# Kernel optimization log

Hardware: AMD Instinct MI355X
Metric: run time of the kernel (lower is better)

## Reference

```python
import jax, jax.numpy as jnp
import numpy as np

NUM_HEADS = 16
HEAD_DIM = 128  # hidden_size 2048 / 16 heads


def setup_inputs() -> dict:
    key = jax.random.key(0)
    k1, k2, k3 = jax.random.split(key, 3)
    bsz, seq, hidden = 2, 2048, 2048
    return {
        "query": jax.random.normal(k1, (bsz, seq, hidden), dtype=jnp.float32),
        "key": jax.random.normal(k2, (bsz, seq, hidden), dtype=jnp.float32),
        "value": jax.random.normal(k3, (bsz, seq, hidden), dtype=jnp.float32),
        "attention_mask": jnp.zeros((1, 1, seq, seq), dtype=jnp.float32),
    }


def reference(query, key, value, attention_mask):
    bsz, seq, hidden = query.shape
    h, d = NUM_HEADS, HEAD_DIM
    # (b, s, h*d) -> (b, h, s, d)
    q = query.reshape(bsz, seq, h, d).transpose(0, 2, 1, 3)
    k = key.reshape(bsz, seq, h, d).transpose(0, 2, 1, 3)
    v = value.reshape(bsz, seq, h, d).transpose(0, 2, 1, 3)
    # scores: (b, h, s, s)
    scores = jnp.einsum("bhqd,bhkd->bhqk", q, k) / jnp.sqrt(jnp.float32(d))
    scores = scores + attention_mask
    probs = jax.nn.softmax(scores.astype(jnp.float32), axis=-1).astype(q.dtype)
    out = jnp.einsum("bhqk,bhkd->bhqd", probs, v)
    # (b, h, s, d) -> (b, s, h*d)
    return out.transpose(0, 2, 1, 3).reshape(bsz, seq, hidden)
```

## Files before the change

### kernel.cpp

```cpp
#include <hip/hip_runtime.h>
#include <hip/hip_bf16.h>
#include <math.h>

#define SEQ 2048
#define NH 16
#define HD 128
#define HID 2048
#define KVB 64
#define NKT (SEQ/KVB)
#define QB 128
#define QBLK 64

typedef __attribute__((ext_vector_type(8))) short bf16x8;
typedef __attribute__((ext_vector_type(4))) short bf16x4;
typedef __attribute__((ext_vector_type(4))) float f32x4;
typedef __attribute__((ext_vector_type(16))) float f32x16;
typedef __attribute__((ext_vector_type(2))) unsigned uint2v;

#define SCL2E 0.1275310261f
#define L2E   1.4426950408889634f

__device__ __forceinline__ short f2bf(float x){
  __hip_bfloat16 h = __float2bfloat16(x);
  return *reinterpret_cast<short*>(&h);
}

__device__ __forceinline__ unsigned cvtpk(float lo, float hi){
  unsigned r;
  asm("v_cvt_pk_bf16_f32 %0, %1, %2" : "=v"(r) : "v"(lo), "v"(hi));
  return r;
}

__device__ __forceinline__ void gld_lds16(const void* g, void* l){
  __builtin_amdgcn_global_load_lds((const __attribute__((address_space(1))) void*)g,
                                   (__attribute__((address_space(3))) void*)l, 16, 0, 0);
}

__global__ void mask_scan_k(const float* __restrict__ m, int n4, int* __restrict__ flag){
  int any = 0;
  const float4* m4 = (const float4*)m;
  for (int i = blockIdx.x*blockDim.x + threadIdx.x; i < n4; i += gridDim.x*blockDim.x){
    float4 v = m4[i];
    any |= (v.x != 0.f) | (v.y != 0.f) | (v.z != 0.f) | (v.w != 0.f);
  }
  if (__ballot(any) != 0ull && (threadIdx.x & 63) == 0) atomicOr(flag, 1);
}

__global__ void cvt_qk_k(const float* __restrict__ in, short* __restrict__ out){
  const int n4 = (2*SEQ*HID)/4;
  for (int i = blockIdx.x*blockDim.x + threadIdx.x; i < n4; i += gridDim.x*blockDim.x){
    int i4 = i*4;
    int b   = i4 >> 22;
    int rem = i4 & ((1<<22)-1);
    int s   = rem >> 11;
    int hd  = rem & 2047;
    int h = hd >> 7, d = hd & 127;
    float4 v = *(const float4*)(in + i4);
    bf16x4 o; o[0]=f2bf(v.x); o[1]=f2bf(v.y); o[2]=f2bf(v.z); o[3]=f2bf(v.w);
    *(bf16x4*)(out + ((size_t)((b*NH + h)*SEQ + s))*HD + d) = o;
  }
}

__global__ void cvt_vt_k(const float* __restrict__ Vg, short* __restrict__ Vt){
  __shared__ short T[64*HD];
  const int bh = blockIdx.x >> 5, st = blockIdx.x & 31;
  const int b = bh >> 4, h = bh & 15;
  const int s0 = st*64;
  const int tid = threadIdx.x;
  const float* vp = Vg + ((size_t)(b*SEQ + s0))*HID + h*HD;
  #pragma unroll
  for (int i = 0; i < 8; ++i){
    int idx = tid + i*256;
    int r = idx >> 5, c4 = idx & 31;
    float4 v = *(const float4*)(vp + (size_t)r*HID + c4*4);
    int X = ((r & 7) ^ ((r >> 3) & 7)) << 3;
    bf16x4 o; o[0]=f2bf(v.x); o[1]=f2bf(v.y); o[2]=f2bf(v.z); o[3]=f2bf(v.w);
    *(bf16x4*)(&T[r*HD + ((c4*4) ^ X)]) = o;
  }
  __syncthreads();
  short* op = Vt + ((size_t)bh*HD)*SEQ + s0;
  #pragma unroll
  for (int u = 0; u < 4; ++u){
    int unit = tid + u*256;
    int sb = unit & 7, d = unit >> 3;
    bf16x8 pk;
    #pragma unroll
    for (int j = 0; j < 8; ++j)
      pk[j] = T[(sb*8 + j)*HD + (d ^ (((j ^ sb) & 7) << 3))];
    *(bf16x8*)(op + (size_t)d*SEQ + sb*8) = pk;
  }
}

__launch_bounds__(256, 2)
__global__ void attn32_k(const float* __restrict__ Qg, const short* __restrict__ Kb,
                         const short* __restrict__ Vtb, const float* __restrict__ Mg,
                         float* __restrict__ Og, const int* __restrict__ flagp)
{
  __shared__ __align__(16) short Kl[2][KVB*HD];
  __shared__ __align__(16) short Vl[2][HD*KVB];

  const int tid = threadIdx.x;
  const int w = tid >> 6, lane = tid & 63;
  const int l31 = lane & 31, hi1 = lane >> 5;
  const int swz = (lane & 7) << 3;

  int bid = blockIdx.x;
  bid = (bid & 7)*64 + (bid >> 3);
  const int bh = bid >> 4;
  const int qt = bid & 15;
  const int b = bh >> 4, h = bh & 15;
  const int mflag = *flagp;
  const int qrow_g = qt*QB + w*32 + l31;

  const short* kbase = Kb + (size_t)bh*SEQ*HD;
  const short* vbase = Vtb + (size_t)bh*HD*SEQ;
  int koff[4], voff[4], cdst[4];
  #pragma unroll
  for (int c = 0; c < 4; ++c){
    int p = (c*4 + w)*1024 + lane*16;
    cdst[c] = (c*4 + w)*1024;
    int r  = p >> 8;
    int cs = (p & 255) >> 1;
    koff[c] = r*HD + (cs ^ ((r & 7) << 3));
    int d   = p >> 7;
    int cs2 = (p & 127) >> 1;
    voff[c] = d*SEQ + (cs2 ^ ((d & 7) << 3));
  }
  auto stage = [&](int bufi, int kt){
    const short* ks = kbase + kt*(KVB*HD);
    const short* vs = vbase + kt*KVB;
    char* kl = (char*)&Kl[bufi][0];
    char* vl = (char*)&Vl[bufi][0];
    #pragma unroll
    for (int c = 0; c < 4; ++c){
      gld_lds16(ks + koff[c], kl + cdst[c]);
      gld_lds16(vs + voff[c], vl + cdst[c]);
    }
  };

  stage(0, 0);

  bf16x8 qf[8];
  {
    const float* qrow = Qg + ((size_t)(b*SEQ + qrow_g))*HID + h*HD;
    #pragma unroll
    for (int ks = 0; ks < 8; ++ks){
      float4 a = *(const float4*)(qrow + ks*16 + hi1*8);
      float4 c = *(const float4*)(qrow + ks*16 + hi1*8 + 4);
      bf16x8 q;
      q[0]=f2bf(a.x); q[1]=f2bf(a.y); q[2]=f2bf(a.z); q[3]=f2bf(a.w);
      q[4]=f2bf(c.x); q[5]=f2bf(c.y); q[6]=f2bf(c.z); q[7]=f2bf(c.w);
      qf[ks] = q;
    }
  }

  f32x16 acc[4];
  #pragma unroll
  for (int cb = 0; cb < 4; ++cb)
    #pragma unroll
    for (int i = 0; i < 16; ++i) acc[cb][i] = 0.f;
  float m_ = -INFINITY, l_ = 0.f;

  asm volatile("s_waitcnt vmcnt(0)" ::: "memory");
  __syncthreads();

  int buf = 0;
  for (int kt = 0; kt < NKT; ++kt){
    if (kt + 1 < NKT) stage(buf^1, kt+1);

    const short* Kc = &Kl[buf][0];
    const short* Vc = &Vl[buf][0];

    f32x16 sv0, sv1;
    #pragma unroll
    for (int i = 0; i < 16; ++i){ sv0[i] = 0.f; sv1[i] = 0.f; }
    const short* krow0 = Kc + l31*HD;
    __builtin_amdgcn_s_setprio(1);
    #pragma unroll
    for (int ks = 0; ks < 8; ++ks){
      int o = (ks*16 + hi1*8) ^ swz;
      bf16x8 kf0 = *(const bf16x8*)(krow0 + o);
      bf16x8 kf1 = *(const bf16x8*)(krow0 + 32*HD + o);
      sv0 = __builtin_amdgcn_mfma_f32_32x32x16_bf16(kf0, qf[ks], sv0, 0, 0, 0);
      sv1 = __builtin_amdgcn_mfma_f32_32x32x16_bf16(kf1, qf[ks], sv1, 0, 0, 0);
    }
    __builtin_amdgcn_s_setprio(0);

    float p[32];
    if (mflag){
      const float* mrow = Mg + (size_t)qrow_g*SEQ + kt*KVB;
      #pragma unroll
      for (int i = 0; i < 16; ++i){
        int kv0 = (i&3) + 8*(i>>2) + 4*hi1;
        p[i]    = sv0[i]*SCL2E + mrow[kv0]*L2E;
        p[16+i] = sv1[i]*SCL2E + mrow[32+kv0]*L2E;
      }
    } else {
      #pragma unroll
      for (int i = 0; i < 16; ++i){ p[i] = sv0[i]*SCL2E; p[16+i] = sv1[i]*SCL2E; }
    }

    float pm = p[0];
    #pragma unroll
    for (int i = 1; i < 32; ++i) pm = fmaxf(pm, p[i]);
    {
      uint2v r = __builtin_amdgcn_permlane32_swap(__float_as_uint(pm), __float_as_uint(pm), false, false);
      pm = fmaxf(__uint_as_float(r[0]), __uint_as_float(r[1]));
    }
    float mn = fmaxf(m_, pm);
    if (!__all(pm - m_ <= 8.0f)){
      float fac = exp2f(m_ - mn);
      m_ = mn; l_ *= fac;
      #pragma unroll
      for (int cb = 0; cb < 4; ++cb)
        #pragma unroll
        for (int i = 0; i < 16; ++i) acc[cb][i] *= fac;
    }
    float rs = 0.f;
    #pragma unroll
    for (int i = 0; i < 32; ++i){ float e = exp2f(p[i] - m_); p[i] = e; rs += e; }
    {
      uint2v r = __builtin_amdgcn_permlane32_swap(__float_as_uint(rs), __float_as_uint(rs), false, false);
      rs = __uint_as_float(r[0]) + __uint_as_float(r[1]);
    }
    l_ += rs;

    bf16x8 pa[4];
    #pragma unroll
    for (int sl = 0; sl < 4; ++sl){
      const int ib = 8*(sl & 1) + 16*(sl >> 1);
      unsigned A0 = cvtpk(p[ib+0], p[ib+1]);
      unsigned A1 = cvtpk(p[ib+2], p[ib+3]);
      unsigned B0 = cvtpk(p[ib+4], p[ib+5]);
      unsigned B1 = cvtpk(p[ib+6], p[ib+7]);
      uint2v r0 = __builtin_amdgcn_permlane32_swap(A0, B0, false, false);
      uint2v r1 = __builtin_amdgcn_permlane32_swap(A1, B1, false, false);
      union { unsigned u[4]; bf16x8 v; } t;
      t.u[0] = r0[0]; t.u[1] = r1[0]; t.u[2] = r0[1]; t.u[3] = r1[1];
      pa[sl] = t.v;
    }

    __builtin_amdgcn_s_setprio(1);
    #pragma unroll
    for (int sl = 0; sl < 4; ++sl){
      int o = (sl*16 + hi1*8) ^ swz;
      #pragma unroll
      for (int cb = 0; cb < 4; ++cb){
        bf16x8 vf = *(const bf16x8*)(Vc + (cb*32 + l31)*KVB + o);
        acc[cb] = __builtin_amdgcn_mfma_f32_32x32x16_bf16(vf, pa[sl], acc[cb], 0, 0, 0);
      }
    }
    __builtin_amdgcn_s_setprio(0);

    asm volatile("s_waitcnt vmcnt(0)" ::: "memory");
    __syncthreads();
    buf ^= 1;
  }

  float inv = 1.0f / l_;
  float* orow = Og + ((size_t)(b*SEQ + qrow_g))*HID + h*HD;
  #pragma unroll
  for (int cb = 0; cb < 4; ++cb)
    #pragma unroll
    for (int g = 0; g < 4; ++g){
      float4 o;
      o.x = acc[cb][g*4+0]*inv; o.y = acc[cb][g*4+1]*inv;
      o.z = acc[cb][g*4+2]*inv; o.w = acc[cb][g*4+3]*inv;
      *(float4*)(orow + cb*32 + g*8 + 4*hi1) = o;
    }
}

__launch_bounds__(256)
__global__ void attn_f32_k(const float* __restrict__ Qg, const float* __restrict__ Kg,
                           const float* __restrict__ Vg, const float* __restrict__ Mg,
                           float* __restrict__ Og, const int* __restrict__ flagp)
{
  __shared__ __align__(16) short Kl[KVB*HD];
  __shared__ __align__(16) short Vt[HD*KVB];
  __shared__ __align__(16) short Pl[4][16*KVB];

  const int tid  = threadIdx.x;
  const int w    = tid >> 6;
  const int lane = tid & 63;
  const int lo   = lane & 15;
  const int hi   = lane >> 4;

  int bid = blockIdx.x;
  bid = (bid & 7)*128 + (bid >> 3);
  const int bh = bid >> 5;
  const int qt = bid & 31;
  const int b  = bh >> 4;
  const int h  = bh & 15;
  const int mflag = *flagp;

  bf16x8 qf[4];
  {
    const float* qrow = Qg + ((size_t)(b*SEQ + qt*QBLK + w*16 + lo))*HID + h*HD;
    #pragma unroll
    for (int kc = 0; kc < 4; ++kc){
      float4 v0 = *(const float4*)(qrow + kc*32 + hi*8);
      float4 v1 = *(const float4*)(qrow + kc*32 + hi*8 + 4);
      bf16x8 q;
      q[0]=f2bf(v0.x); q[1]=f2bf(v0.y); q[2]=f2bf(v0.z); q[3]=f2bf(v0.w);
      q[4]=f2bf(v1.x); q[5]=f2bf(v1.y); q[6]=f2bf(v1.z); q[7]=f2bf(v1.w);
      qf[kc] = q;
    }
  }

  f32x4 acc[8];
  #pragma unroll
  for (int i = 0; i < 8; ++i){ acc[i][0]=0.f; acc[i][1]=0.f; acc[i][2]=0.f; acc[i][3]=0.f; }
  float mrow[4] = {-INFINITY, -INFINITY, -INFINITY, -INFINITY};
  float lrow[4] = {0.f, 0.f, 0.f, 0.f};

  const float* kb = Kg + ((size_t)b*SEQ)*HID + h*HD;
  const float* vb = Vg + ((size_t)b*SEQ)*HID + h*HD;

  for (int kt = 0; kt < NKT; ++kt){
    __syncthreads();
    {
      const float* kp = kb + (size_t)(kt*KVB)*HID;
      #pragma unroll
      for (int i = 0; i < 8; ++i){
        int idx = tid + i*256;
        int r  = idx >> 5;
        int c4 = idx & 31;
        float4 v = *(const float4*)(kp + (size_t)r*HID + c4*4);
        int sidx = (r*HD + c4*4) ^ ((r & 7) << 3);
        short* dst = &Kl[sidx];
        dst[0]=f2bf(v.x); dst[1]=f2bf(v.y); dst[2]=f2bf(v.z); dst[3]=f2bf(v.w);
      }
      const float* vp = vb + (size_t)(kt*KVB)*HID;
      #pragma unroll
      for (int u = 0; u < 4; ++u){
        int unit = tid + u*256;
        int d   = unit & 127;
        int g   = unit >> 7;
        int kv0 = g*8;
        bf16x8 pk;
        #pragma unroll
        for (int j = 0; j < 8; ++j)
          pk[j] = f2bf(vp[(size_t)(kv0 + j)*HID + d]);
        int sidx = (d*KVB + kv0) ^ ((d & 7) << 3);
        *(bf16x8*)(&Vt[sidx]) = pk;
      }
    }
    __syncthreads();

    f32x4 sv[4];
    #pragma unroll
    for (int nb = 0; nb < 4; ++nb){ sv[nb][0]=0.f; sv[nb][1]=0.f; sv[nb][2]=0.f; sv[nb][3]=0.f; }
    #pragma unroll
    for (int nb = 0; nb < 4; ++nb){
      int krow = nb*16 + lo;
      #pragma unroll
      for (int kc = 0; kc < 4; ++kc){
        int sidx = (krow*HD + kc*32 + hi*8) ^ ((krow & 7) << 3);
        bf16x8 kf = *(const bf16x8*)(&Kl[sidx]);
        sv[nb] = __builtin_amdgcn_mfma_f32_16x16x32_bf16(qf[kc], kf, sv[nb], 0, 0, 0);
      }
    }

    float p[4][4];
    if (mflag){
      #pragma unroll
      for (int nb = 0; nb < 4; ++nb)
        #pragma unroll
        for (int r = 0; r < 4; ++r){
          float mv = Mg[(size_t)(qt*QBLK + w*16 + hi*4 + r)*SEQ + kt*KVB + nb*16 + lo];
          p[nb][r] = sv[nb][r]*SCL2E + mv*L2E;
        }
    } else {
      #pragma unroll
      for (int nb = 0; nb < 4; ++nb)
        #pragma unroll
        for (int r = 0; r < 4; ++r)
          p[nb][r] = sv[nb][r]*SCL2E;
    }

    #pragma unroll
    for (int r = 0; r < 4; ++r){
      float mx = fmaxf(fmaxf(p[0][r], p[1][r]), fmaxf(p[2][r], p[3][r]));
      mx = fmaxf(mx, __shfl_xor(mx, 1, 64));
      mx = fmaxf(mx, __shfl_xor(mx, 2, 64));
      mx = fmaxf(mx, __shfl_xor(mx, 4, 64));
      mx = fmaxf(mx, __shfl_xor(mx, 8, 64));
      float mn  = fmaxf(mrow[r], mx);
      float fac = exp2f(mrow[r] - mn);
      mrow[r] = mn;
      lrow[r] *= fac;
      #pragma unroll
      for (int oc = 0; oc < 8; ++oc) acc[oc][r] *= fac;
      float rsv = 0.f;
      #pragma unroll
      for (int nb = 0; nb < 4; ++nb){
        float e = exp2f(p[nb][r] - mn);
        p[nb][r] = e;
        rsv += e;
      }
      rsv += __shfl_xor(rsv, 1, 64);
      rsv += __shfl_xor(rsv, 2, 64);
      rsv += __shfl_xor(rsv, 4, 64);
      rsv += __shfl_xor(rsv, 8, 64);
      lrow[r] += rsv;
    }

    short* myP = &Pl[w][0];
    #pragma unroll
    for (int nb = 0; nb < 4; ++nb)
      #pragma unroll
      for (int r = 0; r < 4; ++r){
        int row = hi*4 + r;
        int sidx = (row*KVB + nb*16 + lo) ^ ((row & 7) << 3);
        myP[sidx] = f2bf(p[nb][r]);
      }

    #pragma unroll
    for (int kc2 = 0; kc2 < 2; ++kc2){
      int sA = (lo*KVB + kc2*32 + hi*8) ^ ((lo & 7) << 3);
      bf16x8 pa = *(const bf16x8*)(&myP[sA]);
      #pragma unroll
      for (int oc = 0; oc < 8; ++oc){
        int vrow = oc*16 + lo;
        int sB = (vrow*KVB + kc2*32 + hi*8) ^ ((vrow & 7) << 3);
        bf16x8 vf = *(const bf16x8*)(&Vt[sB]);
        acc[oc] = __builtin_amdgcn_mfma_f32_16x16x32_bf16(pa, vf, acc[oc], 0, 0, 0);
      }
    }
  }

  float* orow = Og + ((size_t)(b*SEQ + qt*QBLK + w*16))*HID + h*HD;
  #pragma unroll
  for (int r = 0; r < 4; ++r){
    float inv = 1.0f / lrow[r];
    #pragma unroll
    for (int oc = 0; oc < 8; ++oc)
      orow[(size_t)(hi*4 + r)*HID + oc*16 + lo] = acc[oc][r]*inv;
  }
}

extern "C" void kernel_launch(void* const* d_in, const int* in_sizes, int n_in,
                              void* d_out, int out_size, void* d_ws, size_t ws_size,
                              hipStream_t stream)
{
  const float* Qg = (const float*)d_in[0];
  const float* Kg = (const float*)d_in[1];
  const float* Vg = (const float*)d_in[2];
  const float* Mg = (const float*)d_in[3];
  float* Og = (float*)d_out;
  int* flag = (int*)d_ws;

  const size_t plane = (size_t)2*NH*SEQ*HD;
  const size_t need = 64 + 2*plane*sizeof(short);

  hipMemsetAsync(d_ws, 0, 4, stream);
  hipLaunchKernelGGL(mask_scan_k, dim3(256), dim3(256), 0, stream, Mg, SEQ*SEQ/4, flag);

  if (ws_size >= need){
    short* Kb = (short*)((char*)d_ws + 64);
    short* Vt = Kb + plane;
    hipLaunchKernelGGL(cvt_qk_k, dim3(2048), dim3(256), 0, stream, Kg, Kb);
    hipLaunchKernelGGL(cvt_vt_k, dim3(1024), dim3(256), 0, stream, Vg, Vt);
    hipLaunchKernelGGL(attn32_k, dim3(512), dim3(256), 0, stream, Qg, Kb, Vt, Mg, Og, flag);
  } else {
    hipLaunchKernelGGL(attn_f32_k, dim3(32*32), dim3(256), 0, stream, Qg, Kg, Vg, Mg, Og, flag);
  }
}
```

Measured before the change: 134.5 us.

## Drop LDS staging; load K and V fragments directly from global into registers

Removes the shared-memory double buffer and the per-tile barriers in the attention kernel. K fragments are now prefetched from global memory into registers one tile ahead, and V fragments are read directly from global memory inside the PV MFMA loop. The row max and row sum are also changed from serial chains to tree reductions. Each of the four waves now fetches K and V on its own, which means redundant global/L2 traffic and exposed load latency on V, plus more register pressure.

```diff
diff --git a/kernel.cpp b/kernel.cpp
--- a/kernel.cpp
+++ b/kernel.cpp
@@ -29,11 +29,6 @@
   unsigned r;
   asm("v_cvt_pk_bf16_f32 %0, %1, %2" : "=v"(r) : "v"(lo), "v"(hi));
   return r;
-}
-
-__device__ __forceinline__ void gld_lds16(const void* g, void* l){
-  __builtin_amdgcn_global_load_lds((const __attribute__((address_space(1))) void*)g,
-                                   (__attribute__((address_space(3))) void*)l, 16, 0, 0);
 }
 
 __global__ void mask_scan_k(const float* __restrict__ m, int n4, int* __restrict__ flag){
@@ -92,17 +87,13 @@
 }
 
 __launch_bounds__(256, 2)
-__global__ void attn32_k(const float* __restrict__ Qg, const short* __restrict__ Kb,
-                         const short* __restrict__ Vtb, const float* __restrict__ Mg,
-                         float* __restrict__ Og, const int* __restrict__ flagp)
+__global__ void attn_nl_k(const float* __restrict__ Qg, const short* __restrict__ Kbp,
+                          const short* __restrict__ Vtb, const float* __restrict__ Mg,
+                          float* __restrict__ Og, const int* __restrict__ flagp)
 {
-  __shared__ __align__(16) short Kl[2][KVB*HD];
-  __shared__ __align__(16) short Vl[2][HD*KVB];
-
   const int tid = threadIdx.x;
   const int w = tid >> 6, lane = tid & 63;
   const int l31 = lane & 31, hi1 = lane >> 5;
-  const int swz = (lane & 7) << 3;
 
   int bid = blockIdx.x;
   bid = (bid & 7)*64 + (bid >> 3);
@@ -112,34 +103,6 @@
   const int mflag = *flagp;
   const int qrow_g = qt*QB + w*32 + l31;
 
-  const short* kbase = Kb + (size_t)bh*SEQ*HD;
-  const short* vbase = Vtb + (size_t)bh*HD*SEQ;
-  int koff[4], voff[4], cdst[4];
-  #pragma unroll
-  for (int c = 0; c < 4; ++c){
-    int p = (c*4 + w)*1024 + lane*16;
-    cdst[c] = (c*4 + w)*1024;
-    int r  = p >> 8;
-    int cs = (p & 255) >> 1;
-    koff[c] = r*HD + (cs ^ ((r & 7) << 3));
-    int d   = p >> 7;
-    int cs2 = (p & 127) >> 1;
-    voff[c] = d*SEQ + (cs2 ^ ((d & 7) << 3));
-  }
-  auto stage = [&](int bufi, int kt){
-    const short* ks = kbase + kt*(KVB*HD);
-    const short* vs = vbase + kt*KVB;
-    char* kl = (char*)&Kl[bufi][0];
-    char* vl = (char*)&Vl[bufi][0];
-    #pragma unroll
-    for (int c = 0; c < 4; ++c){
-      gld_lds16(ks + koff[c], kl + cdst[c]);
-      gld_lds16(vs + voff[c], vl + cdst[c]);
-    }
-  };
-
-  stage(0, 0);
-
   bf16x8 qf[8];
   {
     const float* qrow = Qg + ((size_t)(b*SEQ + qrow_g))*HID + h*HD;
@@ -154,6 +117,9 @@
     }
   }
 
+  const short* k0base = Kbp + ((size_t)bh*SEQ + l31)*HD + hi1*8;
+  const short* v0base = Vtb + ((size_t)bh*HD + l31)*SEQ + hi1*8;
+
   f32x16 acc[4];
   #pragma unroll
   for (int cb = 0; cb < 4; ++cb)
@@ -161,30 +127,34 @@
     for (int i = 0; i < 16; ++i) acc[cb][i] = 0.f;
   float m_ = -INFINITY, l_ = 0.f;
 
-  asm volatile("s_waitcnt vmcnt(0)" ::: "memory");
-  __syncthreads();
-
-  int buf = 0;
+  bf16x8 kf0[8], kf1[8];
+  #pragma unroll
+  for (int ks = 0; ks < 8; ++ks){
+    kf0[ks] = *(const bf16x8*)(k0base + ks*16);
+    kf1[ks] = *(const bf16x8*)(k0base + 32*HD + ks*16);
+  }
+
   for (int kt = 0; kt < NKT; ++kt){
-    if (kt + 1 < NKT) stage(buf^1, kt+1);
-
-    const short* Kc = &Kl[buf][0];
-    const short* Vc = &Vl[buf][0];
-
     f32x16 sv0, sv1;
     #pragma unroll
     for (int i = 0; i < 16; ++i){ sv0[i] = 0.f; sv1[i] = 0.f; }
-    const short* krow0 = Kc + l31*HD;
     __builtin_amdgcn_s_setprio(1);
     #pragma unroll
     for (int ks = 0; ks < 8; ++ks){
-      int o = (ks*16 + hi1*8) ^ swz;
-      bf16x8 kf0 = *(const bf16x8*)(krow0 + o);
-      bf16x8 kf1 = *(const bf16x8*)(krow0 + 32*HD + o);
-      sv0 = __builtin_amdgcn_mfma_f32_32x32x16_bf16(kf0, qf[ks], sv0, 0, 0, 0);
-      sv1 = __builtin_amdgcn_mfma_f32_32x32x16_bf16(kf1, qf[ks], sv1, 0, 0, 0);
+      sv0 = __builtin_amdgcn_mfma_f32_32x32x16_bf16(kf0[ks], qf[ks], sv0, 0, 0, 0);
+      sv1 = __builtin_amdgcn_mfma_f32_32x32x16_bf16(kf1[ks], qf[ks], sv1, 0, 0, 0);
     }
     __builtin_amdgcn_s_setprio(0);
+
+    {
+      const int ktn = (kt + 1 < NKT) ? kt + 1 : kt;
+      const short* kn = k0base + (size_t)ktn*(KVB*HD);
+      #pragma unroll
+      for (int ks = 0; ks < 8; ++ks){
+        kf0[ks] = *(const bf16x8*)(kn + ks*16);
+        kf1[ks] = *(const bf16x8*)(kn + 32*HD + ks*16);
+      }
+    }
 
     float p[32];
     if (mflag){
@@ -200,10 +170,18 @@
       for (int i = 0; i < 16; ++i){ p[i] = sv0[i]*SCL2E; p[16+i] = sv1[i]*SCL2E; }
     }
 
-    float pm = p[0];
-    #pragma unroll
-    for (int i = 1; i < 32; ++i) pm = fmaxf(pm, p[i]);
+    float pm;
     {
+      float t16[16];
+      #pragma unroll
+      for (int i = 0; i < 16; ++i) t16[i] = fmaxf(p[i], p[i+16]);
+      float t8[8];
+      #pragma unroll
+      for (int i = 0; i < 8; ++i) t8[i] = fmaxf(t16[i], t16[i+8]);
+      float t4[4];
+      #pragma unroll
+      for (int i = 0; i < 4; ++i) t4[i] = fmaxf(t8[i], t8[i+4]);
+      pm = fmaxf(fmaxf(t4[0], t4[1]), fmaxf(t4[2], t4[3]));
       uint2v r = __builtin_amdgcn_permlane32_swap(__float_as_uint(pm), __float_as_uint(pm), false, false);
       pm = fmaxf(__uint_as_float(r[0]), __uint_as_float(r[1]));
     }
@@ -216,14 +194,26 @@
         #pragma unroll
         for (int i = 0; i < 16; ++i) acc[cb][i] *= fac;
     }
-    float rs = 0.f;
-    #pragma unroll
-    for (int i = 0; i < 32; ++i){ float e = exp2f(p[i] - m_); p[i] = e; rs += e; }
     {
+      float s16[16];
+      #pragma unroll
+      for (int i = 0; i < 16; ++i){
+        float e0 = exp2f(p[i] - m_);
+        float e1 = exp2f(p[i+16] - m_);
+        p[i] = e0; p[i+16] = e1;
+        s16[i] = e0 + e1;
+      }
+      float s8[8];
+      #pragma unroll
+      for (int i = 0; i < 8; ++i) s8[i] = s16[i] + s16[i+8];
+      float s4[4];
+      #pragma unroll
+      for (int i = 0; i < 4; ++i) s4[i] = s8[i] + s8[i+4];
+      float rs = (s4[0] + s4[1]) + (s4[2] + s4[3]);
       uint2v r = __builtin_amdgcn_permlane32_swap(__float_as_uint(rs), __float_as_uint(rs), false, false);
       rs = __uint_as_float(r[0]) + __uint_as_float(r[1]);
-    }
-    l_ += rs;
+      l_ += rs;
+    }
 
     bf16x8 pa[4];
     #pragma unroll
@@ -240,21 +230,17 @@
       pa[sl] = t.v;
     }
 
+    const int vcol = kt*KVB;
     __builtin_amdgcn_s_setprio(1);
     #pragma unroll
     for (int sl = 0; sl < 4; ++sl){
-      int o = (sl*16 + hi1*8) ^ swz;
       #pragma unroll
       for (int cb = 0; cb < 4; ++cb){
-        bf16x8 vf = *(const bf16x8*)(Vc + (cb*32 + l31)*KVB + o);
+        bf16x8 vf = *(const bf16x8*)(v0base + (size_t)(cb*32)*SEQ + vcol + sl*16);
         acc[cb] = __builtin_amdgcn_mfma_f32_32x32x16_bf16(vf, pa[sl], acc[cb], 0, 0, 0);
       }
     }
     __builtin_amdgcn_s_setprio(0);
-
-    asm volatile("s_waitcnt vmcnt(0)" ::: "memory");
-    __syncthreads();
-    buf ^= 1;
   }
 
   float inv = 1.0f / l_;
@@ -461,7 +447,7 @@
     short* Vt = Kb + plane;
     hipLaunchKernelGGL(cvt_qk_k, dim3(2048), dim3(256), 0, stream, Kg, Kb);
     hipLaunchKernelGGL(cvt_vt_k, dim3(1024), dim3(256), 0, stream, Vg, Vt);
-    hipLaunchKernelGGL(attn32_k, dim3(512), dim3(256), 0, stream, Qg, Kb, Vt, Mg, Og, flag);
+    hipLaunchKernelGGL(attn_nl_k, dim3(512), dim3(256), 0, stream, Qg, Kb, Vt, Mg, Og, flag);
   } else {
     hipLaunchKernelGGL(attn_f32_k, dim3(32*32), dim3(256), 0, stream, Qg, Kg, Vg, Mg, Og, flag);
   }
```

New measurement: 270.2 us. 101% more time.

## Software-pipeline QK^T of next tile with softmax and PV of current tile

Applied to the files above, without the earlier changes.

Restructures the attention main loop so the QK^T MFMAs for tile t+1 are issued while softmax and the PV product for tile t run, with separate K and V staging (K prefetched two tiles ahead) and split barriers. The softmax scale is folded into Q at load time, and the max and sum reductions become tree-shaped to shorten dependency chains. This aims to hide softmax VALU latency behind matrix work, at the cost of more live registers (two score buffers) and trickier vmcnt and barrier accounting. Folding the scale into Q before the bf16 cast changes rounding slightly.

```diff
diff --git a/kernel.cpp b/kernel.cpp
--- a/kernel.cpp
+++ b/kernel.cpp
@@ -92,9 +92,9 @@
 }
 
 __launch_bounds__(256, 2)
-__global__ void attn32_k(const float* __restrict__ Qg, const short* __restrict__ Kb,
-                         const short* __restrict__ Vtb, const float* __restrict__ Mg,
-                         float* __restrict__ Og, const int* __restrict__ flagp)
+__global__ void attn_p5_k(const float* __restrict__ Qg, const short* __restrict__ Kbp,
+                          const short* __restrict__ Vtb, const float* __restrict__ Mg,
+                          float* __restrict__ Og, const int* __restrict__ flagp)
 {
   __shared__ __align__(16) short Kl[2][KVB*HD];
   __shared__ __align__(16) short Vl[2][HD*KVB];
@@ -112,7 +112,21 @@
   const int mflag = *flagp;
   const int qrow_g = qt*QB + w*32 + l31;
 
-  const short* kbase = Kb + (size_t)bh*SEQ*HD;
+  bf16x8 qf[8];
+  {
+    const float* qrow = Qg + ((size_t)(b*SEQ + qrow_g))*HID + h*HD;
+    #pragma unroll
+    for (int ks = 0; ks < 8; ++ks){
+      float4 a = *(const float4*)(qrow + ks*16 + hi1*8);
+      float4 c = *(const float4*)(qrow + ks*16 + hi1*8 + 4);
+      bf16x8 q;
+      q[0]=f2bf(a.x*SCL2E); q[1]=f2bf(a.y*SCL2E); q[2]=f2bf(a.z*SCL2E); q[3]=f2bf(a.w*SCL2E);
+      q[4]=f2bf(c.x*SCL2E); q[5]=f2bf(c.y*SCL2E); q[6]=f2bf(c.z*SCL2E); q[7]=f2bf(c.w*SCL2E);
+      qf[ks] = q;
+    }
+  }
+
+  const short* kbase = Kbp + (size_t)bh*SEQ*HD;
   const short* vbase = Vtb + (size_t)bh*HD*SEQ;
   int koff[4], voff[4], cdst[4];
   #pragma unroll
@@ -126,33 +140,18 @@
     int cs2 = (p & 127) >> 1;
     voff[c] = d*SEQ + (cs2 ^ ((d & 7) << 3));
   }
-  auto stage = [&](int bufi, int kt){
+  auto stageK = [&](int kt){
     const short* ks = kbase + kt*(KVB*HD);
+    char* kl = (char*)&Kl[kt & 1][0];
+    #pragma unroll
+    for (int c = 0; c < 4; ++c) gld_lds16(ks + koff[c], kl + cdst[c]);
+  };
+  auto stageV = [&](int kt){
     const short* vs = vbase + kt*KVB;
-    char* kl = (char*)&Kl[bufi][0];
-    char* vl = (char*)&Vl[bufi][0];
-    #pragma unroll
-    for (int c = 0; c < 4; ++c){
-      gld_lds16(ks + koff[c], kl + cdst[c]);
-      gld_lds16(vs + voff[c], vl + cdst[c]);
-    }
+    char* vl = (char*)&Vl[kt & 1][0];
+    #pragma unroll
+    for (int c = 0; c < 4; ++c) gld_lds16(vs + voff[c], vl + cdst[c]);
   };
-
-  stage(0, 0);
-
-  bf16x8 qf[8];
-  {
-    const float* qrow = Qg + ((size_t)(b*SEQ + qrow_g))*HID + h*HD;
-    #pragma unroll
-    for (int ks = 0; ks < 8; ++ks){
-      float4 a = *(const float4*)(qrow + ks*16 + hi1*8);
-      float4 c = *(const float4*)(qrow + ks*16 + hi1*8 + 4);
-      bf16x8 q;
-      q[0]=f2bf(a.x); q[1]=f2bf(a.y); q[2]=f2bf(a.z); q[3]=f2bf(a.w);
-      q[4]=f2bf(c.x); q[5]=f2bf(c.y); q[6]=f2bf(c.z); q[7]=f2bf(c.w);
-      qf[ks] = q;
-    }
-  }
 
   f32x16 acc[4];
   #pragma unroll
@@ -161,101 +160,131 @@
     for (int i = 0; i < 16; ++i) acc[cb][i] = 0.f;
   float m_ = -INFINITY, l_ = 0.f;
 
-  asm volatile("s_waitcnt vmcnt(0)" ::: "memory");
-  __syncthreads();
-
-  int buf = 0;
-  for (int kt = 0; kt < NKT; ++kt){
-    if (kt + 1 < NKT) stage(buf^1, kt+1);
-
-    const short* Kc = &Kl[buf][0];
-    const short* Vc = &Vl[buf][0];
-
-    f32x16 sv0, sv1;
-    #pragma unroll
-    for (int i = 0; i < 16; ++i){ sv0[i] = 0.f; sv1[i] = 0.f; }
-    const short* krow0 = Kc + l31*HD;
+  auto qkt = [&](int kt, f32x16& s0, f32x16& s1){
+    const short* Kc = &Kl[kt & 1][0];
+    f32x16 a0, a1;
+    #pragma unroll
+    for (int i = 0; i < 16; ++i){ a0[i] = 0.f; a1[i] = 0.f; }
     __builtin_amdgcn_s_setprio(1);
     #pragma unroll
     for (int ks = 0; ks < 8; ++ks){
       int o = (ks*16 + hi1*8) ^ swz;
-      bf16x8 kf0 = *(const bf16x8*)(krow0 + o);
-      bf16x8 kf1 = *(const bf16x8*)(krow0 + 32*HD + o);
-      sv0 = __builtin_amdgcn_mfma_f32_32x32x16_bf16(kf0, qf[ks], sv0, 0, 0, 0);
-      sv1 = __builtin_amdgcn_mfma_f32_32x32x16_bf16(kf1, qf[ks], sv1, 0, 0, 0);
+      bf16x8 kf0 = *(const bf16x8*)(Kc + l31*HD + o);
+      bf16x8 kf1 = *(const bf16x8*)(Kc + (32 + l31)*HD + o);
+      a0 = __builtin_amdgcn_mfma_f32_32x32x16_bf16(kf0, qf[ks], a0, 0, 0, 0);
+      a1 = __builtin_amdgcn_mfma_f32_32x32x16_bf16(kf1, qf[ks], a1, 0, 0, 0);
     }
     __builtin_amdgcn_s_setprio(0);
-
-    float p[32];
-    if (mflag){
-      const float* mrow = Mg + (size_t)qrow_g*SEQ + kt*KVB;
-      #pragma unroll
-      for (int i = 0; i < 16; ++i){
-        int kv0 = (i&3) + 8*(i>>2) + 4*hi1;
-        p[i]    = sv0[i]*SCL2E + mrow[kv0]*L2E;
-        p[16+i] = sv1[i]*SCL2E + mrow[32+kv0]*L2E;
-      }
-    } else {
-      #pragma unroll
-      for (int i = 0; i < 16; ++i){ p[i] = sv0[i]*SCL2E; p[16+i] = sv1[i]*SCL2E; }
-    }
-
-    float pm = p[0];
-    #pragma unroll
-    for (int i = 1; i < 32; ++i) pm = fmaxf(pm, p[i]);
-    {
-      uint2v r = __builtin_amdgcn_permlane32_swap(__float_as_uint(pm), __float_as_uint(pm), false, false);
-      pm = fmaxf(__uint_as_float(r[0]), __uint_as_float(r[1]));
-    }
-    float mn = fmaxf(m_, pm);
-    if (!__all(pm - m_ <= 8.0f)){
-      float fac = exp2f(m_ - mn);
-      m_ = mn; l_ *= fac;
-      #pragma unroll
-      for (int cb = 0; cb < 4; ++cb)
-        #pragma unroll
-        for (int i = 0; i < 16; ++i) acc[cb][i] *= fac;
-    }
-    float rs = 0.f;
-    #pragma unroll
-    for (int i = 0; i < 32; ++i){ float e = exp2f(p[i] - m_); p[i] = e; rs += e; }
-    {
-      uint2v r = __builtin_amdgcn_permlane32_swap(__float_as_uint(rs), __float_as_uint(rs), false, false);
-      rs = __uint_as_float(r[0]) + __uint_as_float(r[1]);
-    }
-    l_ += rs;
-
-    bf16x8 pa[4];
-    #pragma unroll
-    for (int sl = 0; sl < 4; ++sl){
-      const int ib = 8*(sl & 1) + 16*(sl >> 1);
-      unsigned A0 = cvtpk(p[ib+0], p[ib+1]);
-      unsigned A1 = cvtpk(p[ib+2], p[ib+3]);
-      unsigned B0 = cvtpk(p[ib+4], p[ib+5]);
-      unsigned B1 = cvtpk(p[ib+6], p[ib+7]);
-      uint2v r0 = __builtin_amdgcn_permlane32_swap(A0, B0, false, false);
-      uint2v r1 = __builtin_amdgcn_permlane32_swap(A1, B1, false, false);
-      union { unsigned u[4]; bf16x8 v; } t;
-      t.u[0] = r0[0]; t.u[1] = r1[0]; t.u[2] = r0[1]; t.u[3] = r1[1];
-      pa[sl] = t.v;
-    }
-
-    __builtin_amdgcn_s_setprio(1);
-    #pragma unroll
-    for (int sl = 0; sl < 4; ++sl){
-      int o = (sl*16 + hi1*8) ^ swz;
-      #pragma unroll
-      for (int cb = 0; cb < 4; ++cb){
-        bf16x8 vf = *(const bf16x8*)(Vc + (cb*32 + l31)*KVB + o);
-        acc[cb] = __builtin_amdgcn_mfma_f32_32x32x16_bf16(vf, pa[sl], acc[cb], 0, 0, 0);
-      }
-    }
-    __builtin_amdgcn_s_setprio(0);
-
-    asm volatile("s_waitcnt vmcnt(0)" ::: "memory");
-    __syncthreads();
-    buf ^= 1;
-  }
+    s0 = a0; s1 = a1;
+  };
+
+  stageK(0); stageV(0); stageK(1);
+  asm volatile("s_waitcnt vmcnt(8)" ::: "memory");
+  __builtin_amdgcn_s_barrier();
+  f32x16 svE0, svE1, svO0, svO1;
+  qkt(0, svE0, svE1);
+
+#define SUBSTEP(T, C0, C1, N0, N1, DOSV, DOSK, VMC, DOQ, DOBAR) do {              \
+    if (DOSV) stageV((T)+1);                                                      \
+    if (DOSK) stageK((T)+2);                                                      \
+    float p[32];                                                                  \
+    if (mflag){                                                                   \
+      const float* mrow = Mg + (size_t)qrow_g*SEQ + (T)*KVB;                      \
+      _Pragma("unroll")                                                           \
+      for (int i = 0; i < 16; ++i){                                               \
+        int kv0 = (i&3) + 8*(i>>2) + 4*hi1;                                       \
+        p[i]    = C0[i] + mrow[kv0]*L2E;                                          \
+        p[16+i] = C1[i] + mrow[32+kv0]*L2E;                                       \
+      }                                                                           \
+    } else {                                                                      \
+      _Pragma("unroll")                                                           \
+      for (int i = 0; i < 16; ++i){ p[i] = C0[i]; p[16+i] = C1[i]; }              \
+    }                                                                             \
+    asm volatile("s_waitcnt vmcnt(" VMC ")" ::: "memory");                        \
+    __builtin_amdgcn_s_barrier();                                                 \
+    if (DOQ) qkt((T)+1, N0, N1);                                                  \
+    float pm;                                                                     \
+    {                                                                             \
+      float t16[16];                                                              \
+      _Pragma("unroll")                                                           \
+      for (int i = 0; i < 16; ++i) t16[i] = fmaxf(p[i], p[i+16]);                 \
+      float t8[8];                                                                \
+      _Pragma("unroll")                                                           \
+      for (int i = 0; i < 8; ++i) t8[i] = fmaxf(t16[i], t16[i+8]);                \
+      float t4[4];                                                                \
+      _Pragma("unroll")                                                           \
+      for (int i = 0; i < 4; ++i) t4[i] = fmaxf(t8[i], t8[i+4]);                  \
+      pm = fmaxf(fmaxf(t4[0], t4[1]), fmaxf(t4[2], t4[3]));                       \
+      uint2v rr = __builtin_amdgcn_permlane32_swap(__float_as_uint(pm), __float_as_uint(pm), false, false); \
+      pm = fmaxf(__uint_as_float(rr[0]), __uint_as_float(rr[1]));                 \
+    }                                                                             \
+    float mn = fmaxf(m_, pm);                                                     \
+    if (!__all(pm - m_ <= 8.0f)){                                                 \
+      float fac = exp2f(m_ - mn);                                                 \
+      m_ = mn; l_ *= fac;                                                         \
+      _Pragma("unroll")                                                           \
+      for (int cb = 0; cb < 4; ++cb)                                              \
+        _Pragma("unroll")                                                         \
+        for (int i = 0; i < 16; ++i) acc[cb][i] *= fac;                           \
+    }                                                                             \
+    {                                                                             \
+      float s16[16];                                                              \
+      _Pragma("unroll")                                                           \
+      for (int i = 0; i < 16; ++i){                                               \
+        float e0 = exp2f(p[i] - m_);                                              \
+        float e1 = exp2f(p[i+16] - m_);                                           \
+        p[i] = e0; p[i+16] = e1;                                                  \
+        s16[i] = e0 + e1;                                                         \
+      }                                                                           \
+      float s8[8];                                                                \
+      _Pragma("unroll")                                                           \
+      for (int i = 0; i < 8; ++i) s8[i] = s16[i] + s16[i+8];                      \
+      float s4[4];                                                                \
+      _Pragma("unroll")                                                           \
+      for (int i = 0; i < 4; ++i) s4[i] = s8[i] + s8[i+4];                        \
+      float rs = (s4[0] + s4[1]) + (s4[2] + s4[3]);                               \
+      uint2v rr = __builtin_amdgcn_permlane32_swap(__float_as_uint(rs), __float_as_uint(rs), false, false); \
+      rs = __uint_as_float(rr[0]) + __uint_as_float(rr[1]);                       \
+      l_ += rs;                                                                   \
+    }                                                                             \
+    bf16x8 pa[4];                                                                 \
+    _Pragma("unroll")                                                             \
+    for (int sl = 0; sl < 4; ++sl){                                               \
+      const int ib = 8*(sl & 1) + 16*(sl >> 1);                                   \
+      unsigned A0 = cvtpk(p[ib+0], p[ib+1]);                                      \
+      unsigned A1 = cvtpk(p[ib+2], p[ib+3]);                                      \
+      unsigned B0 = cvtpk(p[ib+4], p[ib+5]);                                      \
+      unsigned B1 = cvtpk(p[ib+6], p[ib+7]);                                      \
+      uint2v r0 = __builtin_amdgcn_permlane32_swap(A0, B0, false, false);         \
+      uint2v r1 = __builtin_amdgcn_permlane32_swap(A1, B1, false, false);         \
+      union { unsigned u[4]; bf16x8 v; } tt;                                      \
+      tt.u[0] = r0[0]; tt.u[1] = r1[0]; tt.u[2] = r0[1]; tt.u[3] = r1[1];         \
+      pa[sl] = tt.v;                                                              \
+    }                                                                             \
+    {                                                                             \
+      const short* Vc = &Vl[(T) & 1][0];                                          \
+      __builtin_amdgcn_s_setprio(1);                                              \
+      _Pragma("unroll")                                                           \
+      for (int sl = 0; sl < 4; ++sl){                                             \
+        int o = (sl*16 + hi1*8) ^ swz;                                            \
+        _Pragma("unroll")                                                         \
+        for (int cb = 0; cb < 4; ++cb){                                           \
+          bf16x8 vf = *(const bf16x8*)(Vc + (cb*32 + l31)*KVB + o);               \
+          acc[cb] = __builtin_amdgcn_mfma_f32_32x32x16_bf16(vf, pa[sl], acc[cb], 0, 0, 0); \
+        }                                                                         \
+      }                                                                           \
+      __builtin_amdgcn_s_setprio(0);                                              \
+    }                                                                             \
+    if (DOBAR) __builtin_amdgcn_s_barrier();                                      \
+  } while(0)
+
+  for (int t = 0; t < NKT-2; t += 2){
+    SUBSTEP(t,   svE0, svE1, svO0, svO1, 1, 1, "8", 1, 1);
+    SUBSTEP(t+1, svO0, svO1, svE0, svE1, 1, 1, "8", 1, 1);
+  }
+  SUBSTEP(NKT-2, svE0, svE1, svO0, svO1, 1, 0, "4", 1, 1);
+  SUBSTEP(NKT-1, svO0, svO1, svE0, svE1, 0, 0, "0", 0, 0);
+#undef SUBSTEP
 
   float inv = 1.0f / l_;
   float* orow = Og + ((size_t)(b*SEQ + qrow_g))*HID + h*HD;
@@ -461,7 +490,7 @@
     short* Vt = Kb + plane;
     hipLaunchKernelGGL(cvt_qk_k, dim3(2048), dim3(256), 0, stream, Kg, Kb);
     hipLaunchKernelGGL(cvt_vt_k, dim3(1024), dim3(256), 0, stream, Vg, Vt);
-    hipLaunchKernelGGL(attn32_k, dim3(512), dim3(256), 0, stream, Qg, Kb, Vt, Mg, Og, flag);
+    hipLaunchKernelGGL(attn_p5_k, dim3(512), dim3(256), 0, stream, Qg, Kb, Vt, Mg, Og, flag);
   } else {
     hipLaunchKernelGGL(attn_f32_k, dim3(32*32), dim3(256), 0, stream, Qg, Kg, Vg, Mg, Og, flag);
   }
```

New measurement: 132.2 us. No clear change (-1.7%).
